# Kernel optimization log

Hardware: AMD Instinct MI355X
Metric: run time of the kernel (lower is better)

## Reference

```python
import jax, jax.numpy as jnp
import numpy as np

B = 5                      # dat_sz hardcoded in module; kernel shapes force batch == 5
X_DIM = 4096
H_DIM = 4096
T_DIM = 4096
D_DIM = X_DIM // T_DIM     # = 1 (required so z_dim == t_dim broadcasts in reparameterize_nm)
L_DIM = D_DIM * (D_DIM + 1) // 2
Z_DIM = T_DIM * L_DIM      # = 4096


def _linear_params(key, din, dout):
    kw, kb = jax.random.split(key)
    W = jax.random.normal(kw, (din, dout), dtype=jnp.float32) / np.float32(np.sqrt(din))
    b = jax.random.normal(kb, (dout,), dtype=jnp.float32) * np.float32(0.01)
    return W, b


def setup_inputs() -> dict:
    key = jax.random.key(0)
    ks = jax.random.split(key, 20)
    inp = {}
    inp["x"] = jax.random.normal(ks[0], (B, X_DIM), dtype=jnp.float32)
    inp["eps_xi"] = jax.random.normal(ks[1], (B, T_DIM), dtype=jnp.float32)
    inp["eps_f"] = jax.random.normal(ks[2], (B, D_DIM), dtype=jnp.float32)
    inp["eps_z"] = jax.random.normal(ks[3], (B, Z_DIM), dtype=jnp.float32)
    inp["W1"], inp["b1"] = _linear_params(ks[4], X_DIM, H_DIM)
    inp["W11"], inp["b11"] = _linear_params(ks[5], H_DIM, T_DIM)
    inp["W12"], inp["b12"] = _linear_params(ks[6], H_DIM, T_DIM)
    inp["W2"], inp["b2"] = _linear_params(ks[7], D_DIM, H_DIM)
    inp["W21"], inp["b21"] = _linear_params(ks[8], H_DIM, Z_DIM)
    inp["W22"], inp["b22"] = _linear_params(ks[9], H_DIM, T_DIM)
    inp["W23"], inp["b23"] = _linear_params(ks[10], X_DIM + Z_DIM, H_DIM)
    inp["W24"], inp["b24"] = _linear_params(ks[11], H_DIM, T_DIM + D_DIM)
    inp["W25"], inp["b25"] = _linear_params(ks[12], H_DIM, T_DIM + D_DIM)
    inp["W3"], inp["b3"] = _linear_params(ks[13], Z_DIM, H_DIM)
    inp["W31"], inp["b31"] = _linear_params(ks[14], H_DIM, X_DIM)
    inp["W32"], inp["b32"] = _linear_params(ks[15], H_DIM, X_DIM)
    inp["s"] = jax.random.normal(ks[16], (B, T_DIM), dtype=jnp.float32)
    inp["t"] = jax.random.normal(ks[17], (B, D_DIM), dtype=jnp.float32)
    inp["sigma"] = jnp.asarray(0.01, dtype=jnp.float32)
    inp["w"] = jnp.ones((T_DIM,), dtype=jnp.float32) / np.float32(T_DIM)
    inp["dist"] = 1  # unused by forward (matches torch signature)
    return inp


def _ard_kernel(a, b, sigma, w):
    # K[i,j] = sigma^2 * exp(-0.5 * sum_d w_d (a_i,d - b_j,d)^2)
    # Vectorized replacement of the original O(B^2) Python double loop.
    d2 = (a[:, None, :] - b[None, :, :]) ** 2            # [B, B, T]
    return (sigma ** 2) * jnp.exp(-0.5 * jnp.einsum('ijt,t->ij', d2, w))


def reference(x, eps_xi, eps_f, eps_z,
              W1, b1, W11, b11, W12, b12,
              W2, b2, W21, b21, W22, b22,
              W23, b23, W24, b24, W25, b25,
              W3, b3, W31, b31, W32, b32,
              s, t, sigma, w, dist):
    relu = jax.nn.relu
    # encode_1
    h1 = relu(x @ W1 + b1)
    qxi_mean = h1 @ W11 + b11
    log_qxi_cov = h1 @ W12 + b12
    # reparameterize_nm
    xi = jnp.exp(0.5 * log_qxi_cov) * eps_xi + qxi_mean
    # reparameterize_gp (training branch)
    K_ss = _ard_kernel(s, s, sigma, w)                    # [5,5]
    K_xs = _ard_kernel(xi, s, sigma, w)                   # [5,5]
    kk_inv = K_xs @ jnp.linalg.inv(K_ss)                  # [5,5]
    qf_mean = kk_inv @ t                                  # [5,D]
    cov = _ard_kernel(xi, xi, sigma, w) - kk_inv @ _ard_kernel(s, xi, sigma, w)
    qf_cov = jnp.diag(cov)                                # [5]
    f = jnp.sqrt(qf_cov)[:, None] * eps_f + qf_mean       # [5,D]
    # encode_2
    h2 = relu(f @ W2 + b2)
    z_mean = h2 @ W21 + b21                               # [5,Z]
    z_cov = h2 @ W22 + b22                                # [5,T] (== Z since d_dim=1)
    z = jnp.exp(0.5 * z_cov) * eps_z + z_mean
    # encode_3
    h23 = relu(jnp.concatenate([x, z], axis=1) @ W23 + b23)
    r_mean = h23 @ W24 + b24                              # [5,T+D]
    r_cov = h23 @ W25 + b25
    # decode
    h3 = relu(z @ W3 + b3)
    x_mean = h3 @ W31 + b31
    x_cov = h3 @ W32 + b32
    # losses
    qf_cov2 = jnp.broadcast_to(qf_cov[:, None], (B, D_DIM))
    q_mean = jnp.concatenate([qxi_mean, qf_mean], axis=1)
    q_cov = jnp.concatenate([log_qxi_cov, jnp.log(qf_cov2)], axis=1)
    kld1 = 0.5 * jnp.sum(-z_cov - 1.0 + jnp.exp(z_cov) + z_mean ** 2) / B
    kld2 = 0.5 * jnp.sum(r_cov - q_cov - 1.0
                         + jnp.exp(q_cov - r_cov)
                         + (q_mean - r_mean) ** 2 * jnp.exp(-r_cov)) / B
    kld_loss = kld1 + kld2
    log_pi = jnp.log(jnp.asarray(np.pi, dtype=jnp.float32))
    nll_loss = 0.5 * jnp.sum(log_pi + x_cov + jnp.exp(-x_cov) * (x - x_mean) ** 2) / B
    return (kld_loss, nll_loss, z_mean, z_cov, x_mean, x_cov)
```

## Files before the change

### kernel.cpp

```cpp
#include <hip/hip_runtime.h>
#include <math.h>

#define B5 5
#define DX 4096
#define DT 4096
#define DR 4097

enum {
  WS_SUMS  = 0,
  WS_CNT_XI  = 3,
  WS_CNT_FIN = 4,
  WS_CNT_ARD = 5,
  WS_ZERO_END = 8,
  WS_ACT1  = 16,
  WS_ACT23 = WS_ACT1  + 20480,
  WS_ACT3  = WS_ACT23 + 20480,
  WS_QXI_F = WS_ACT3  + 20480,
  WS_LQC_F = WS_QXI_F + 20480,
  WS_XIV   = WS_LQC_F + 20480,
  WS_Z     = WS_XIV   + 20480,
  WS_KSS   = WS_Z     + 20480,
  WS_KXS   = WS_KSS + 32,
  WS_F     = WS_KXS + 32,
  WS_QFM   = WS_F   + 8,
  WS_QFC   = WS_QFM + 8,
  WS_PART  = 143472,
  WS_P_H1  = WS_PART,
  WS_P_QXI = WS_P_H1  + 1310720,
  WS_P_LQC = WS_P_QXI + 1310720,
  WS_P_ZM  = WS_P_LQC + 1310720,
  WS_P_ZC  = WS_P_ZM  + 1310720,
  WS_P_H23 = WS_P_ZC  + 1310720,
  WS_P_H3  = WS_P_H23 + 2621440,
  WS_P_RM  = WS_P_H3  + 1310720,
  WS_P_RC  = WS_P_RM  + 1311040,
  WS_P_XM  = WS_P_RC  + 1311040,
  WS_P_XC  = WS_P_XM  + 1310720,
  WS_END   = WS_P_XC  + 1310720
};

#define GCOLS 128
#define GK    64
#define WROWS 16

typedef float f2v __attribute__((ext_vector_type(2)));

__device__ inline float wave_sum(float v) {
  #pragma unroll
  for (int o = 32; o > 0; o >>= 1) v += __shfl_down(v, o, 64);
  return v;
}

template<int PROLOG, int DUAL, int ALIGNED>
__device__ __forceinline__ void gemm5_body(
    float* sx, float* red, int bx, int by,
    const float* __restrict__ p0, const float* __restrict__ p1,
    const float* __restrict__ p2,
    const float* __restrict__ Wa, const float* __restrict__ Wb,
    float* __restrict__ Pa,       float* __restrict__ Pb,
    int din, int dout)
{
  const int tid  = threadIdx.x;
  const int lane = tid & 63;
  const int wv   = tid >> 6;
  const long i0  = (long)by * GK;
  const long r0  = i0 + (long)wv * WROWS;

  float* sw = sx + wv * 80;
  for (int t = lane; t < B5 * WROWS; t += 64) {
    int b  = t >> 4;
    int il = t & 15;
    int i  = (int)(r0 + il);
    float v;
    if (PROLOG == 0)      v = p0[(long)b * din + i];
    else if (PROLOG == 2) v = fmaxf(p0[b] * p1[i] + p2[i], 0.f);
    else                  v = (i < DX) ? p0[(long)b * DX + i] : p1[(long)b * DT + (i - DX)];
    sw[t] = v;
  }

  const long o0 = (long)bx * GCOLS + lane * 2;
  const bool v0 = (o0 < dout);
  const bool v1 = (o0 + 1 < dout);

  float accA[B5][2] = {};
  float accB[B5][2] = {};
  const float* wa = Wa + r0 * dout + o0;
  const float* wb = DUAL ? (Wb + r0 * dout + o0) : nullptr;

  #pragma unroll 8
  for (int il = 0; il < WROWS; ++il) {
    float w0a, w1a, w0b = 0.f, w1b = 0.f;
    if (ALIGNED) {
      f2v ta = __builtin_nontemporal_load((const f2v*)wa);
      w0a = ta.x; w1a = ta.y;
      if (DUAL) {
        f2v tb = __builtin_nontemporal_load((const f2v*)wb);
        w0b = tb.x; w1b = tb.y;
      }
    } else {
      w0a = v0 ? __builtin_nontemporal_load(wa) : 0.f;
      w1a = v1 ? __builtin_nontemporal_load(wa + 1) : 0.f;
      if (DUAL) {
        w0b = v0 ? __builtin_nontemporal_load(wb) : 0.f;
        w1b = v1 ? __builtin_nontemporal_load(wb + 1) : 0.f;
      }
    }
    #pragma unroll
    for (int b = 0; b < B5; ++b) {
      float xv = sw[b * WROWS + il];
      accA[b][0] += xv * w0a; accA[b][1] += xv * w1a;
      if (DUAL) { accB[b][0] += xv * w0b; accB[b][1] += xv * w1b; }
    }
    wa += dout; if (DUAL) wb += dout;
  }

  const int NJ = DUAL ? 20 : 10;
  if (wv > 0) {
    float* rr = red + (long)(wv - 1) * NJ * 64 + lane;
    #pragma unroll
    for (int b = 0; b < B5; ++b) {
      rr[(b*2)*64] = accA[b][0]; rr[(b*2+1)*64] = accA[b][1];
      if (DUAL) { rr[(10+b*2)*64] = accB[b][0]; rr[(10+b*2+1)*64] = accB[b][1]; }
    }
  }
  __syncthreads();
  if (wv == 0) {
    #pragma unroll
    for (int w2 = 0; w2 < 3; ++w2) {
      const float* rr = red + (long)w2 * NJ * 64 + lane;
      #pragma unroll
      for (int b = 0; b < B5; ++b) {
        accA[b][0] += rr[(b*2)*64]; accA[b][1] += rr[(b*2+1)*64];
        if (DUAL) { accB[b][0] += rr[(10+b*2)*64]; accB[b][1] += rr[(10+b*2+1)*64]; }
      }
    }
    if (v0) {
      #pragma unroll
      for (int b = 0; b < B5; ++b) {
        float* pa = Pa + ((long)by * B5 + b) * dout + o0;
        if (ALIGNED) *(float2*)pa = make_float2(accA[b][0], accA[b][1]);
        else { pa[0] = accA[b][0]; if (v1) pa[1] = accA[b][1]; }
        if (DUAL) {
          float* pb = Pb + ((long)by * B5 + b) * dout + o0;
          if (ALIGNED) *(float2*)pb = make_float2(accB[b][0], accB[b][1]);
          else { pb[0] = accB[b][0]; if (v1) pb[1] = accB[b][1]; }
        }
      }
    }
  }
}

template<int PROLOG, int DUAL, int ALIGNED>
__global__ __launch_bounds__(256) void gemm5(
    const float* __restrict__ p0, const float* __restrict__ p1,
    const float* __restrict__ p2,
    const float* __restrict__ Wa, const float* __restrict__ Wb,
    float* __restrict__ Pa,       float* __restrict__ Pb,
    int din, int dout)
{
  __shared__ float sx[4 * 80];
  __shared__ float red[3 * 20 * 64];
  gemm5_body<PROLOG, DUAL, ALIGNED>(sx, red, blockIdx.x, blockIdx.y,
      p0, p1, p2, Wa, Wb, Pa, Pb, din, dout);
}

__global__ __launch_bounds__(256) void gemm5_G46(
    const float* __restrict__ x,   const float* __restrict__ z,
    const float* __restrict__ W23, float* __restrict__ P23,
    const float* __restrict__ W3,  float* __restrict__ P3)
{
  __shared__ float sx[4 * 80];
  __shared__ float red[3 * 20 * 64];
  int id = blockIdx.x;
  if (id < 4096) {
    gemm5_body<3, 0, 1>(sx, red, id & 31, id >> 5, x, z, nullptr,
                        W23, nullptr, P23, nullptr, 8192, 4096);
  } else {
    id -= 4096;
    gemm5_body<0, 0, 1>(sx, red, id & 31, id >> 5, z, nullptr, nullptr,
                        W3, nullptr, P3, nullptr, 4096, 4096);
  }
}

__global__ __launch_bounds__(256) void gemm5_G57(
    const float* __restrict__ act23,
    const float* __restrict__ W24, const float* __restrict__ W25,
    float* __restrict__ PRM,       float* __restrict__ PRC,
    const float* __restrict__ act3,
    const float* __restrict__ W31, const float* __restrict__ W32,
    float* __restrict__ PXM,       float* __restrict__ PXC)
{
  __shared__ float sx[4 * 80];
  __shared__ float red[3 * 20 * 64];
  int id = blockIdx.x;
  if (id < 2112) {
    gemm5_body<0, 1, 0>(sx, red, id % 33, id / 33, act23, nullptr, nullptr,
                        W24, W25, PRM, PRC, 4096, 4097);
  } else {
    id -= 2112;
    gemm5_body<0, 1, 1>(sx, red, id & 31, id >> 5, act3, nullptr, nullptr,
                        W31, W32, PXM, PXC, 4096, 4096);
  }
}

__global__ __launch_bounds__(256) void k_act1(
    const float* __restrict__ P, const float* __restrict__ bias, float* __restrict__ act,
    float* __restrict__ ctrl)
{
  if (blockIdx.x == 0 && threadIdx.x < WS_ZERO_END) ctrl[threadIdx.x] = 0.f;
  int idx = blockIdx.x * 256 + threadIdx.x;
  int b = idx >> 12, col = idx & (DT - 1);
  const float* pp = P + (long)b * DT + col;
  float s = 0.f;
  #pragma unroll 8
  for (int ks = 0; ks < 64; ++ks) s += pp[(long)ks * (B5 * DT)];
  act[idx] = fmaxf(s + bias[col], 0.f);
}

__global__ __launch_bounds__(256) void k_act23(
    const float* __restrict__ P23, const float* __restrict__ b23, float* __restrict__ act23,
    const float* __restrict__ P3,  const float* __restrict__ b3,  float* __restrict__ act3)
{
  int idx = blockIdx.x * 256 + threadIdx.x;
  if (idx < B5 * DT) {
    int b = idx >> 12, col = idx & (DT - 1);
    const float* pp = P23 + (long)b * DT + col;
    float s = 0.f;
    #pragma unroll 8
    for (int ks = 0; ks < 128; ++ks) s += pp[(long)ks * (B5 * DT)];
    act23[idx] = fmaxf(s + b23[col], 0.f);
  } else {
    int j = idx - B5 * DT;
    int b = j >> 12, col = j & (DT - 1);
    const float* pp = P3 + (long)b * DT + col;
    float s = 0.f;
    #pragma unroll 8
    for (int ks = 0; ks < 64; ++ks) s += pp[(long)ks * (B5 * DT)];
    act3[j] = fmaxf(s + b3[col], 0.f);
  }
}

__global__ __launch_bounds__(256) void k_xi(
    const float* __restrict__ Pq, const float* __restrict__ Pl,
    const float* __restrict__ b11, const float* __restrict__ b12,
    const float* __restrict__ eps_xi,
    float* __restrict__ qf, float* __restrict__ lf, float* __restrict__ xiv)
{
  int idx = blockIdx.x * 256 + threadIdx.x;
  if (idx >= B5 * DT) return;
  int b = idx >> 12, col = idx & (DT - 1);
  const float* pq = Pq + (long)b * DT + col;
  const float* pl = Pl + (long)b * DT + col;
  float sq = 0.f, sl = 0.f;
  #pragma unroll 8
  for (int ks = 0; ks < 64; ++ks) { sq += pq[(long)ks * (B5 * DT)]; sl += pl[(long)ks * (B5 * DT)]; }
  float qm = sq + b11[col];
  float lq = sl + b12[col];
  qf[idx] = qm; lf[idx] = lq;
  xiv[idx] = expf(0.5f * lq) * eps_xi[idx] + qm;
}

__global__ __launch_bounds__(256) void k_ardgp(
    const float* __restrict__ s,    const float* __restrict__ xiv,
    const float* __restrict__ w,    const float* __restrict__ sigma,
    const float* __restrict__ t_in, const float* __restrict__ eps_f,
    float* __restrict__ Kss, float* __restrict__ Kxs, int* __restrict__ cnt,
    float* __restrict__ fv, float* __restrict__ qfm, float* __restrict__ qfc)
{
  const int bid = blockIdx.x;
  const bool xs = (bid >= 25);
  int q = xs ? bid - 25 : bid;
  const int i = q / 5, j = q % 5;
  const float* aa = xs ? (xiv + (long)i * DT) : (s + (long)i * DT);
  const float* bb = s + (long)j * DT;

  float sum = 0.f;
  for (int t = threadIdx.x; t < DT; t += 256) {
    float d = aa[t] - bb[t];
    sum += w[t] * d * d;
  }
  sum = wave_sum(sum);
  __shared__ float red[4];
  int lane = threadIdx.x & 63, wv = threadIdx.x >> 6;
  if (lane == 0) red[wv] = sum;
  __syncthreads();

  if (threadIdx.x == 0) {
    float tot = red[0] + red[1] + red[2] + red[3];
    float sg = sigma[0];
    float K = sg * sg * expf(-0.5f * tot);
    (xs ? Kxs : Kss)[i * 5 + j] = K;
    __threadfence();
    int old = atomicAdd(cnt, 1);
    if (old == 49) {
      __threadfence();
      double M[5][5], Inv[5][5];
      for (int a = 0; a < 5; ++a)
        for (int b = 0; b < 5; ++b) { M[a][b] = Kss[a * 5 + b]; Inv[a][b] = (a == b) ? 1.0 : 0.0; }
      for (int c = 0; c < 5; ++c) {
        int p = c; double best = fabs(M[c][c]);
        for (int r = c + 1; r < 5; ++r) if (fabs(M[r][c]) > best) { best = fabs(M[r][c]); p = r; }
        if (p != c)
          for (int k = 0; k < 5; ++k) {
            double tm = M[c][k]; M[c][k] = M[p][k]; M[p][k] = tm;
            tm = Inv[c][k]; Inv[c][k] = Inv[p][k]; Inv[p][k] = tm;
          }
        double piv = 1.0 / M[c][c];
        for (int k = 0; k < 5; ++k) { M[c][k] *= piv; Inv[c][k] *= piv; }
        for (int r = 0; r < 5; ++r) if (r != c) {
          double m = M[r][c];
          for (int k = 0; k < 5; ++k) { M[r][k] -= m * M[c][k]; Inv[r][k] -= m * Inv[c][k]; }
        }
      }
      double kk[5][5];
      for (int a = 0; a < 5; ++a)
        for (int b = 0; b < 5; ++b) {
          double acc = 0.0;
          for (int k = 0; k < 5; ++k) acc += (double)Kxs[a * 5 + k] * Inv[k][b];
          kk[a][b] = acc;
        }
      double sg2 = (double)sg * (double)sg;
      for (int a = 0; a < 5; ++a) {
        double qm = 0.0, qc = sg2;
        for (int b = 0; b < 5; ++b) { qm += kk[a][b] * (double)t_in[b]; qc -= kk[a][b] * (double)Kxs[a * 5 + b]; }
        if (qc < 1e-12) qc = 1e-12;
        qfm[a] = (float)qm;
        qfc[a] = (float)qc;
        fv[a]  = sqrtf((float)qc) * eps_f[a] + (float)qm;
      }
    }
  }
}

__global__ __launch_bounds__(256) void k_z(
    const float* __restrict__ Pm, const float* __restrict__ Pc,
    const float* __restrict__ b21, const float* __restrict__ b22,
    const float* __restrict__ eps_z,
    float* __restrict__ out_zm, float* __restrict__ out_zc,
    float* __restrict__ zv, float* __restrict__ kld1sum)
{
  int idx = blockIdx.x * 256 + threadIdx.x;
  float term = 0.f;
  if (idx < B5 * DT) {
    int b = idx >> 12, col = idx & (DT - 1);
    const float* pm = Pm + (long)b * DT + col;
    const float* pc = Pc + (long)b * DT + col;
    float sm = 0.f, sc = 0.f;
    #pragma unroll 8
    for (int ks = 0; ks < 64; ++ks) { sm += pm[(long)ks * (B5 * DT)]; sc += pc[(long)ks * (B5 * DT)]; }
    float zm = sm + b21[col];
    float zc = sc + b22[col];
    out_zm[idx] = zm; out_zc[idx] = zc;
    zv[idx] = expf(0.5f * zc) * eps_z[idx] + zm;
    term = -zc - 1.f + expf(zc) + zm * zm;
  }
  term = wave_sum(term);
  if ((threadIdx.x & 63) == 0) atomicAdd(kld1sum, term);
}

__global__ __launch_bounds__(256) void k_fin(
    const float* __restrict__ Prm, const float* __restrict__ Prc,
    const float* __restrict__ b24, const float* __restrict__ b25,
    const float* __restrict__ qxi, const float* __restrict__ lqc,
    const float* __restrict__ qfm, const float* __restrict__ qfc,
    const float* __restrict__ Pxm, const float* __restrict__ Pxc,
    const float* __restrict__ b31, const float* __restrict__ b32,
    const float* __restrict__ x,
    float* __restrict__ out_xm, float* __restrict__ out_xc,
    float* __restrict__ sums, int* __restrict__ cnt, float* __restrict__ out01)
{
  const int gtid = blockIdx.x * 256 + threadIdx.x;
  float t2 = 0.f, t3 = 0.f;
  if (gtid < B5 * DR) {
    int b = gtid / DR, col = gtid % DR;
    const float* pm = Prm + (long)b * DR + col;
    const float* pc = Prc + (long)b * DR + col;
    float sm = 0.f, sc = 0.f;
    #pragma unroll 8
    for (int ks = 0; ks < 64; ++ks) { sm += pm[(long)ks * (B5 * DR)]; sc += pc[(long)ks * (B5 * DR)]; }
    float rm = sm + b24[col];
    float rc = sc + b25[col];
    float qm, qc;
    if (col < DT) { qm = qxi[(long)b * DT + col]; qc = lqc[(long)b * DT + col]; }
    else          { qm = qfm[b]; qc = logf(qfc[b]); }
    float d = qm - rm;
    t2 = rc - qc - 1.f + expf(qc - rc) + d * d * expf(-rc);
  } else {
    int idx = gtid - B5 * DR;
    if (idx < B5 * DX) {
      int b = idx >> 12, col = idx & (DX - 1);
      const float* pm = Pxm + (long)b * DX + col;
      const float* pc = Pxc + (long)b * DX + col;
      float sm = 0.f, sc = 0.f;
      #pragma unroll 8
      for (int ks = 0; ks < 64; ++ks) { sm += pm[(long)ks * (B5 * DX)]; sc += pc[(long)ks * (B5 * DX)]; }
      float xm = sm + b31[col];
      float xc = sc + b32[col];
      out_xm[idx] = xm; out_xc[idx] = xc;
      float d = x[idx] - xm;
      t3 = 1.14472988584940017f + xc + expf(-xc) * d * d;
    }
  }
  t2 = wave_sum(t2);
  t3 = wave_sum(t3);
  if ((threadIdx.x & 63) == 0) {
    if (t2 != 0.f) atomicAdd(&sums[1], t2);
    if (t3 != 0.f) atomicAdd(&sums[2], t3);
  }
  __syncthreads();
  if (threadIdx.x == 0) {
    __threadfence();
    int old = atomicAdd(cnt, 1);
    if (old == (int)gridDim.x - 1) {
      __threadfence();
      out01[0] = 0.5f * (sums[0] + sums[1]) / (float)B5;
      out01[1] = 0.5f * sums[2] / (float)B5;
    }
  }
}

extern "C" void kernel_launch(void* const* d_in, const int* in_sizes, int n_in,
                              void* d_out, int out_size, void* d_ws, size_t ws_size,
                              hipStream_t stream)
{
  const float* x      = (const float*)d_in[0];
  const float* eps_xi = (const float*)d_in[1];
  const float* eps_f  = (const float*)d_in[2];
  const float* eps_z  = (const float*)d_in[3];
  const float* W1  = (const float*)d_in[4];  const float* b1  = (const float*)d_in[5];
  const float* W11 = (const float*)d_in[6];  const float* b11 = (const float*)d_in[7];
  const float* W12 = (const float*)d_in[8];  const float* b12 = (const float*)d_in[9];
  const float* W2  = (const float*)d_in[10]; const float* b2  = (const float*)d_in[11];
  const float* W21 = (const float*)d_in[12]; const float* b21 = (const float*)d_in[13];
  const float* W22 = (const float*)d_in[14]; const float* b22 = (const float*)d_in[15];
  const float* W23 = (const float*)d_in[16]; const float* b23 = (const float*)d_in[17];
  const float* W24 = (const float*)d_in[18]; const float* b24 = (const float*)d_in[19];
  const float* W25 = (const float*)d_in[20]; const float* b25 = (const float*)d_in[21];
  const float* W3  = (const float*)d_in[22]; const float* b3  = (const float*)d_in[23];
  const float* W31 = (const float*)d_in[24]; const float* b31 = (const float*)d_in[25];
  const float* W32 = (const float*)d_in[26]; const float* b32 = (const float*)d_in[27];
  const float* s     = (const float*)d_in[28];
  const float* t     = (const float*)d_in[29];
  const float* sigma = (const float*)d_in[30];
  const float* w     = (const float*)d_in[31];

  float* ws  = (float*)d_ws;
  float* out = (float*)d_out;

  dim3 blk(256);

  gemm5<0,0,1><<<dim3(32,64), blk, 0, stream>>>(
      x, nullptr, nullptr, W1, nullptr, ws + WS_P_H1, nullptr, 4096, 4096);
  k_act1<<<80, blk, 0, stream>>>(ws + WS_P_H1, b1, ws + WS_ACT1, ws);
  gemm5<0,1,1><<<dim3(32,64), blk, 0, stream>>>(
      ws + WS_ACT1, nullptr, nullptr, W11, W12, ws + WS_P_QXI, ws + WS_P_LQC, 4096, 4096);
  k_xi<<<80, blk, 0, stream>>>(
      ws + WS_P_QXI, ws + WS_P_LQC, b11, b12, eps_xi,
      ws + WS_QXI_F, ws + WS_LQC_F, ws + WS_XIV);
  k_ardgp<<<50, blk, 0, stream>>>(
      s, ws + WS_XIV, w, sigma, t, eps_f,
      ws + WS_KSS, ws + WS_KXS, (int*)(ws + WS_CNT_ARD),
      ws + WS_F, ws + WS_QFM, ws + WS_QFC);
  gemm5<2,1,1><<<dim3(32,64), blk, 0, stream>>>(
      ws + WS_F, W2, b2, W21, W22, ws + WS_P_ZM, ws + WS_P_ZC, 4096, 4096);
  k_z<<<80, blk, 0, stream>>>(
      ws + WS_P_ZM, ws + WS_P_ZC, b21, b22, eps_z,
      out + 2, out + 2 + 20480, ws + WS_Z, ws + WS_SUMS);
  gemm5_G46<<<6144, blk, 0, stream>>>(
      x, ws + WS_Z, W23, ws + WS_P_H23, W3, ws + WS_P_H3);
  k_act23<<<160, blk, 0, stream>>>(
      ws + WS_P_H23, b23, ws + WS_ACT23, ws + WS_P_H3, b3, ws + WS_ACT3);
  gemm5_G57<<<4160, blk, 0, stream>>>(
      ws + WS_ACT23, W24, W25, ws + WS_P_RM, ws + WS_P_RC,
      ws + WS_ACT3,  W31, W32, ws + WS_P_XM, ws + WS_P_XC);
  k_fin<<<161, blk, 0, stream>>>(
      ws + WS_P_RM, ws + WS_P_RC, b24, b25,
      ws + WS_QXI_F, ws + WS_LQC_F,
      ws + WS_QFM, ws + WS_QFC,
      ws + WS_P_XM, ws + WS_P_XC, b31, b32, x,
      out + 2 + 40960, out + 2 + 61440,
      ws + WS_SUMS, (int*)(ws + WS_CNT_FIN), out);
}
```

Before: 235.7 us.

## Fuse xi reduction with ARD kernel via spin-wait, use nontemporal partial loads

Merges the xi split-K reduction kernel and the ARD-GP kernel into one launch, using a global counter so the cross-kernel blocks spin until all xi blocks finish. Kss blocks, which do not depend on xi, can start right away. This removes one kernel launch and its gap. Separately, all split-K partial-sum reads now use nontemporal loads to avoid polluting cache. The spin-wait assumes every xi block gets scheduled alongside the waiting blocks, which holds at 130 blocks but is a forward-progress risk.

After: 252.9 us. 1.07x slower.

```diff
diff --git a/kernel.cpp b/kernel.cpp
--- a/kernel.cpp
+++ b/kernel.cpp
@@ -45,6 +45,8 @@
 
 typedef float f2v __attribute__((ext_vector_type(2)));
 
+__device__ inline float ntl(const float* p) { return __builtin_nontemporal_load(p); }
+
 __device__ inline float wave_sum(float v) {
   #pragma unroll
   for (int o = 32; o > 0; o >>= 1) v += __shfl_down(v, o, 64);
@@ -98,11 +100,11 @@
         w0b = tb.x; w1b = tb.y;
       }
     } else {
-      w0a = v0 ? __builtin_nontemporal_load(wa) : 0.f;
-      w1a = v1 ? __builtin_nontemporal_load(wa + 1) : 0.f;
+      w0a = v0 ? ntl(wa) : 0.f;
+      w1a = v1 ? ntl(wa + 1) : 0.f;
       if (DUAL) {
-        w0b = v0 ? __builtin_nontemporal_load(wb) : 0.f;
-        w1b = v1 ? __builtin_nontemporal_load(wb + 1) : 0.f;
+        w0b = v0 ? ntl(wb) : 0.f;
+        w1b = v1 ? ntl(wb + 1) : 0.f;
       }
     }
     #pragma unroll
@@ -213,7 +215,7 @@
   const float* pp = P + (long)b * DT + col;
   float s = 0.f;
   #pragma unroll 8
-  for (int ks = 0; ks < 64; ++ks) s += pp[(long)ks * (B5 * DT)];
+  for (int ks = 0; ks < 64; ++ks) s += ntl(pp + (long)ks * (B5 * DT));
   act[idx] = fmaxf(s + bias[col], 0.f);
 }
 
@@ -227,7 +229,7 @@
     const float* pp = P23 + (long)b * DT + col;
     float s = 0.f;
     #pragma unroll 8
-    for (int ks = 0; ks < 128; ++ks) s += pp[(long)ks * (B5 * DT)];
+    for (int ks = 0; ks < 128; ++ks) s += ntl(pp + (long)ks * (B5 * DT));
     act23[idx] = fmaxf(s + b23[col], 0.f);
   } else {
     int j = idx - B5 * DT;
@@ -235,42 +237,54 @@
     const float* pp = P3 + (long)b * DT + col;
     float s = 0.f;
     #pragma unroll 8
-    for (int ks = 0; ks < 64; ++ks) s += pp[(long)ks * (B5 * DT)];
+    for (int ks = 0; ks < 64; ++ks) s += ntl(pp + (long)ks * (B5 * DT));
     act3[j] = fmaxf(s + b3[col], 0.f);
   }
 }
 
-__global__ __launch_bounds__(256) void k_xi(
+__global__ __launch_bounds__(256) void k_xiard(
     const float* __restrict__ Pq, const float* __restrict__ Pl,
     const float* __restrict__ b11, const float* __restrict__ b12,
     const float* __restrict__ eps_xi,
-    float* __restrict__ qf, float* __restrict__ lf, float* __restrict__ xiv)
-{
-  int idx = blockIdx.x * 256 + threadIdx.x;
-  if (idx >= B5 * DT) return;
-  int b = idx >> 12, col = idx & (DT - 1);
-  const float* pq = Pq + (long)b * DT + col;
-  const float* pl = Pl + (long)b * DT + col;
-  float sq = 0.f, sl = 0.f;
-  #pragma unroll 8
-  for (int ks = 0; ks < 64; ++ks) { sq += pq[(long)ks * (B5 * DT)]; sl += pl[(long)ks * (B5 * DT)]; }
-  float qm = sq + b11[col];
-  float lq = sl + b12[col];
-  qf[idx] = qm; lf[idx] = lq;
-  xiv[idx] = expf(0.5f * lq) * eps_xi[idx] + qm;
-}
-
-__global__ __launch_bounds__(256) void k_ardgp(
-    const float* __restrict__ s,    const float* __restrict__ xiv,
-    const float* __restrict__ w,    const float* __restrict__ sigma,
+    const float* __restrict__ s,   const float* __restrict__ w,
+    const float* __restrict__ sigma,
     const float* __restrict__ t_in, const float* __restrict__ eps_f,
-    float* __restrict__ Kss, float* __restrict__ Kxs, int* __restrict__ cnt,
+    float* __restrict__ qf, float* __restrict__ lf, float* __restrict__ xiv,
+    float* __restrict__ Kss, float* __restrict__ Kxs,
+    int* __restrict__ cnt_xi, int* __restrict__ cnt_ard,
     float* __restrict__ fv, float* __restrict__ qfm, float* __restrict__ qfc)
 {
-  const int bid = blockIdx.x;
+  if (blockIdx.x < 80) {
+    int idx = blockIdx.x * 256 + threadIdx.x;
+    int b = idx >> 12, col = idx & (DT - 1);
+    const float* pq = Pq + (long)b * DT + col;
+    const float* pl = Pl + (long)b * DT + col;
+    float sq = 0.f, sl = 0.f;
+    #pragma unroll 8
+    for (int ks = 0; ks < 64; ++ks) {
+      sq += ntl(pq + (long)ks * (B5 * DT));
+      sl += ntl(pl + (long)ks * (B5 * DT));
+    }
+    float qm = sq + b11[col];
+    float lq = sl + b12[col];
+    qf[idx] = qm; lf[idx] = lq;
+    xiv[idx] = expf(0.5f * lq) * eps_xi[idx] + qm;
+    __threadfence();
+    __syncthreads();
+    if (threadIdx.x == 0) atomicAdd(cnt_xi, 1);
+    return;
+  }
+
+  const int bid = blockIdx.x - 80;
   const bool xs = (bid >= 25);
   int q = xs ? bid - 25 : bid;
   const int i = q / 5, j = q % 5;
+
+  if (xs) {
+    if (threadIdx.x == 0) { while (atomicAdd(cnt_xi, 0) < 80) {} }
+    __syncthreads();
+    __threadfence();
+  }
   const float* aa = xs ? (xiv + (long)i * DT) : (s + (long)i * DT);
   const float* bb = s + (long)j * DT;
 
@@ -280,18 +294,18 @@
     sum += w[t] * d * d;
   }
   sum = wave_sum(sum);
-  __shared__ float red[4];
+  __shared__ float red4[4];
   int lane = threadIdx.x & 63, wv = threadIdx.x >> 6;
-  if (lane == 0) red[wv] = sum;
+  if (lane == 0) red4[wv] = sum;
   __syncthreads();
 
   if (threadIdx.x == 0) {
-    float tot = red[0] + red[1] + red[2] + red[3];
+    float tot = red4[0] + red4[1] + red4[2] + red4[3];
     float sg = sigma[0];
     float K = sg * sg * expf(-0.5f * tot);
     (xs ? Kxs : Kss)[i * 5 + j] = K;
     __threadfence();
-    int old = atomicAdd(cnt, 1);
+    int old = atomicAdd(cnt_ard, 1);
     if (old == 49) {
       __threadfence();
       double M[5][5], Inv[5][5];
@@ -347,7 +361,10 @@
     const float* pc = Pc + (long)b * DT + col;
     float sm = 0.f, sc = 0.f;
     #pragma unroll 8
-    for (int ks = 0; ks < 64; ++ks) { sm += pm[(long)ks * (B5 * DT)]; sc += pc[(long)ks * (B5 * DT)]; }
+    for (int ks = 0; ks < 64; ++ks) {
+      sm += ntl(pm + (long)ks * (B5 * DT));
+      sc += ntl(pc + (long)ks * (B5 * DT));
+    }
     float zm = sm + b21[col];
     float zc = sc + b22[col];
     out_zm[idx] = zm; out_zc[idx] = zc;
@@ -377,7 +394,10 @@
     const float* pc = Prc + (long)b * DR + col;
     float sm = 0.f, sc = 0.f;
     #pragma unroll 8
-    for (int ks = 0; ks < 64; ++ks) { sm += pm[(long)ks * (B5 * DR)]; sc += pc[(long)ks * (B5 * DR)]; }
+    for (int ks = 0; ks < 64; ++ks) {
+      sm += ntl(pm + (long)ks * (B5 * DR));
+      sc += ntl(pc + (long)ks * (B5 * DR));
+    }
     float rm = sm + b24[col];
     float rc = sc + b25[col];
     float qm, qc;
@@ -393,7 +413,10 @@
       const float* pc = Pxc + (long)b * DX + col;
       float sm = 0.f, sc = 0.f;
       #pragma unroll 8
-      for (int ks = 0; ks < 64; ++ks) { sm += pm[(long)ks * (B5 * DX)]; sc += pc[(long)ks * (B5 * DX)]; }
+      for (int ks = 0; ks < 64; ++ks) {
+        sm += ntl(pm + (long)ks * (B5 * DX));
+        sc += ntl(pc + (long)ks * (B5 * DX));
+      }
       float xm = sm + b31[col];
       float xc = sc + b32[col];
       out_xm[idx] = xm; out_xc[idx] = xc;
@@ -454,12 +477,12 @@
   k_act1<<<80, blk, 0, stream>>>(ws + WS_P_H1, b1, ws + WS_ACT1, ws);
   gemm5<0,1,1><<<dim3(32,64), blk, 0, stream>>>(
       ws + WS_ACT1, nullptr, nullptr, W11, W12, ws + WS_P_QXI, ws + WS_P_LQC, 4096, 4096);
-  k_xi<<<80, blk, 0, stream>>>(
+  k_xiard<<<130, blk, 0, stream>>>(
       ws + WS_P_QXI, ws + WS_P_LQC, b11, b12, eps_xi,
-      ws + WS_QXI_F, ws + WS_LQC_F, ws + WS_XIV);
-  k_ardgp<<<50, blk, 0, stream>>>(
-      s, ws + WS_XIV, w, sigma, t, eps_f,
-      ws + WS_KSS, ws + WS_KXS, (int*)(ws + WS_CNT_ARD),
+      s, w, sigma, t, eps_f,
+      ws + WS_QXI_F, ws + WS_LQC_F, ws + WS_XIV,
+      ws + WS_KSS, ws + WS_KXS,
+      (int*)(ws + WS_CNT_XI), (int*)(ws + WS_CNT_ARD),
       ws + WS_F, ws + WS_QFM, ws + WS_QFC);
   gemm5<2,1,1><<<dim3(32,64), blk, 0, stream>>>(
       ws + WS_F, W2, b2, W21, W22, ws + WS_P_ZM, ws + WS_P_ZC, 4096, 4096);
```
